# Kernel tuning notes

Measured on AMD Instinct MI355X. Metric: run time of the kernel, lower is better.

The kernel has to match this reference:

```python
import jax, jax.numpy as jnp
import numpy as np

B, S, D, H, HD, L, P = 32, 511, 512, 8, 64, 4, 501
PD = 32
FD = D - 2 * PD  # feature_proj output dim = hidden - 2*player_dim
DFF = 4 * D


def _pe(T, d):
    pos = jnp.arange(T, dtype=jnp.float32)[:, None]
    div = jnp.exp(jnp.arange(0, d, 2, dtype=jnp.float32) * (-np.log(10000.0) / d))
    pe = jnp.zeros((T, d), jnp.float32)
    pe = pe.at[:, 0::2].set(jnp.sin(pos * div))
    pe = pe.at[:, 1::2].set(jnp.cos(pos * div))
    return pe


def _ln(x, g, b, eps=1e-5):
    mu = x.mean(-1, keepdims=True)
    v = jnp.mean((x - mu) ** 2, -1, keepdims=True)
    return (x - mu) * jax.lax.rsqrt(v + eps) * g + b


def _forward(runs, wickets, overs, batters, bowlers, player_embed, Wf, bf,
             query_token, Wq, bq, Wk, bk, Wv, bv, Wo, bo,
             rec_s, bow_s, bat_s, W1, b1, W2, b2, g1, be1, g2, be2, Wout, bout):
    Bt, St = runs.shape
    T = St + 1
    # ball embedding: [B,S,3]@[3,FD] cat player embeds -> [B,S,D]
    feats = jnp.stack([runs, wickets, overs], -1) @ Wf + bf
    x = jnp.concatenate([feats, player_embed[batters], player_embed[bowlers]], -1)
    # append learned query token, add sinusoidal PE
    x = jnp.concatenate([x, jnp.broadcast_to(query_token, (Bt, 1, D))], 1)
    x = x + _pe(T, D)[None]
    # actor masks, padded with ones for the query row/col -> [B,T,T]
    sb = (bowlers[:, :, None] == bowlers[:, None, :]).astype(x.dtype)
    sm = (batters[:, :, None] == batters[:, None, :]).astype(x.dtype)
    row = jnp.ones((Bt, 1, St), x.dtype)
    col = jnp.ones((Bt, T, 1), x.dtype)
    sb = jnp.concatenate([jnp.concatenate([sb, row], 1), col], 2)
    sm = jnp.concatenate([jnp.concatenate([sm, row], 1), col], 2)
    causal = jnp.triu(jnp.ones((T, T), bool), 1)
    rec = jnp.arange(T, dtype=x.dtype) / T  # recency bias over key positions
    scale = 1.0 / np.float32(np.sqrt(HD))
    for l in range(L):
        q = (x @ Wq[l] + bq[l]).reshape(Bt, T, H, HD).transpose(0, 2, 1, 3)
        k = (x @ Wk[l] + bk[l]).reshape(Bt, T, H, HD).transpose(0, 2, 1, 3)
        v = (x @ Wv[l] + bv[l]).reshape(Bt, T, H, HD).transpose(0, 2, 1, 3)
        scores = jnp.einsum('bhqd,bhkd->bhqk', q, k) * scale
        # specialized head biases (num_heads >= 3)
        scores = scores.at[:, 0].add((rec_s[l] * rec)[None, None, :])
        scores = scores.at[:, 1].add(bow_s[l] * sb)
        scores = scores.at[:, 2].add(bat_s[l] * sm)
        scores = jnp.where(causal[None, None], -jnp.inf, scores)
        a = jax.nn.softmax(scores, axis=-1)
        o = jnp.einsum('bhqk,bhkd->bhqd', a, v).transpose(0, 2, 1, 3).reshape(Bt, T, D)
        x = _ln(x + o @ Wo[l] + bo[l], g1[l], be1[l])
        ff = jax.nn.gelu(x @ W1[l] + b1[l], approximate=False) @ W2[l] + b2[l]
        x = _ln(x + ff, g2[l], be2[l])
    return x[:, -1] @ Wout + bout  # [B, D]


def setup_inputs() -> dict:
    key = jax.random.key(0)
    ks = jax.random.split(key, 16)
    w = lambda k, sh: (0.02 * jax.random.normal(k, sh)).astype(jnp.float32)
    return {
        'runs': jax.random.uniform(ks[0], (B, S), jnp.float32),
        'wickets': jax.random.uniform(ks[1], (B, S), jnp.float32),
        'overs': jax.random.uniform(ks[2], (B, S), jnp.float32),
        'batters': jax.random.randint(ks[3], (B, S), 0, 500, jnp.int32),
        'bowlers': jax.random.randint(ks[4], (B, S), 0, 500, jnp.int32),
        'player_embed': w(ks[5], (P, PD)),
        'Wf': w(ks[6], (3, FD)), 'bf': jnp.zeros((FD,), jnp.float32),
        'query_token': jax.random.normal(ks[7], (1, 1, D), jnp.float32),
        'Wq': w(ks[8], (L, D, D)), 'bq': jnp.zeros((L, D), jnp.float32),
        'Wk': w(ks[9], (L, D, D)), 'bk': jnp.zeros((L, D), jnp.float32),
        'Wv': w(ks[10], (L, D, D)), 'bv': jnp.zeros((L, D), jnp.float32),
        'Wo': w(ks[11], (L, D, D)), 'bo': jnp.zeros((L, D), jnp.float32),
        'rec_s': jnp.full((L,), 0.5, jnp.float32),
        'bow_s': jnp.full((L,), 2.0, jnp.float32),
        'bat_s': jnp.full((L,), 2.0, jnp.float32),
        'W1': w(ks[12], (L, D, DFF)), 'b1': jnp.zeros((L, DFF), jnp.float32),
        'W2': w(ks[13], (L, DFF, D)), 'b2': jnp.zeros((L, D), jnp.float32),
        'g1': jnp.ones((L, D), jnp.float32), 'be1': jnp.zeros((L, D), jnp.float32),
        'g2': jnp.ones((L, D), jnp.float32), 'be2': jnp.zeros((L, D), jnp.float32),
        'Wout': w(ks[14], (D, D)), 'bout': jnp.zeros((D,), jnp.float32),
    }


def reference(runs, wickets, overs, batters, bowlers, player_embed, Wf, bf,
              query_token, Wq, bq, Wk, bk, Wv, bv, Wo, bo,
              rec_s, bow_s, bat_s, W1, b1, W2, b2, g1, be1, g2, be2, Wout, bout):
    return _forward(runs, wickets, overs, batters, bowlers, player_embed, Wf, bf,
                    query_token, Wq, bq, Wk, bk, Wv, bv, Wo, bo,
                    rec_s, bow_s, bat_s, W1, b1, W2, b2, g1, be1, g2, be2, Wout, bout)
```

## Files before the change

kernel.cpp:

```cpp
#include <hip/hip_runtime.h>
#include <math.h>

#define B_ 32
#define S_ 511
#define T_ 512
#define D_ 512
#define H_ 8
#define HD_ 64
#define L_ 4
#define P_ 501
#define PD_ 32
#define FD_ 448
#define DFF_ 2048

typedef __attribute__((ext_vector_type(8))) short bf16x8;
typedef __attribute__((ext_vector_type(4))) float f32x4;

__device__ __forceinline__ unsigned short f2bf(float f) {
  union { float f; unsigned int u; } c; c.f = f;
  unsigned int r = c.u + 0x7FFFu + ((c.u >> 16) & 1u);
  return (unsigned short)(r >> 16);
}

__global__ __launch_bounds__(256) void wtrans_kernel(
    const float* __restrict__ in, unsigned short* __restrict__ out, int K, int N)
{
  __shared__ float t[64][65];
  const int l = blockIdx.z;
  in  += (size_t)l * K * N;
  out += (size_t)l * N * K;
  const int k0 = blockIdx.x * 64, n0 = blockIdx.y * 64;
  const int tx = threadIdx.x & 63, ty = threadIdx.x >> 6;
#pragma unroll
  for (int i = 0; i < 16; ++i) {
    int r = ty + i * 4;
    t[r][tx] = in[(size_t)(k0 + r) * N + n0 + tx];
  }
  __syncthreads();
#pragma unroll
  for (int i = 0; i < 16; ++i) {
    int r = ty + i * 4;
    out[(size_t)(n0 + r) * K + k0 + tx] = f2bf(t[tx][r]);
  }
}

__global__ __launch_bounds__(256) void embed_kernel(
    const float* __restrict__ runs, const float* __restrict__ wickets,
    const float* __restrict__ overs, const int* __restrict__ batters,
    const int* __restrict__ bowlers, const float* __restrict__ pemb,
    const float* __restrict__ Wf, const float* __restrict__ bfv,
    const float* __restrict__ qtok, float* __restrict__ x,
    unsigned short* __restrict__ xb)
{
  size_t idx = (size_t)blockIdx.x * 256 + threadIdx.x;
  const size_t total = (size_t)B_ * T_ * D_;
  if (idx >= total) return;
  int d = (int)(idx % D_);
  int t = (int)((idx / D_) % T_);
  int b = (int)(idx / ((size_t)D_ * T_));
  float val;
  if (t < S_) {
    size_t st = (size_t)b * S_ + t;
    if (d < FD_) {
      val = runs[st] * Wf[d] + wickets[st] * Wf[FD_ + d] + overs[st] * Wf[2 * FD_ + d] + bfv[d];
    } else if (d < FD_ + PD_) {
      val = pemb[(size_t)batters[st] * PD_ + (d - FD_)];
    } else {
      val = pemb[(size_t)bowlers[st] * PD_ + (d - FD_ - PD_)];
    }
  } else {
    val = qtok[d];
  }
  float div = expf((float)(2 * (d >> 1)) * (-9.210340371976184f / (float)D_));
  float ang = (float)t * div;
  val += (d & 1) ? cosf(ang) : sinf(ang);
  x[idx] = val;
  xb[idx] = f2bf(val);
}

template<int ACT>
__global__ __launch_bounds__(256) void mfma_gemm(
    const unsigned short* __restrict__ A, const unsigned short* __restrict__ Bt,
    const float* __restrict__ bias, float* __restrict__ C,
    unsigned short* __restrict__ Cb, int N, int K)
{
  __shared__ unsigned short As[128 * 32];
  __shared__ unsigned short Bs[128 * 32];
  const int tid = threadIdx.x;
  const int m0 = blockIdx.y * 128, n0 = blockIdx.x * 128;
  const int lane = tid & 63, w = tid >> 6;
  const int wr = w >> 1, wc = w & 1;
  const int lr = lane & 15, lg = lane >> 4;

  f32x4 acc[4][4] = {};

  const int sr = tid >> 2, sc8 = (tid & 3) * 8;
  const unsigned short* gA = A + (size_t)(m0 + sr) * K + sc8;
  const unsigned short* gB = Bt + (size_t)(n0 + sr) * K + sc8;
  const size_t rowK64 = (size_t)64 * K;

  for (int k0 = 0; k0 < K; k0 += 32) {
    __syncthreads();
    *(bf16x8*)&As[sr * 32 + sc8]        = *(const bf16x8*)(gA + k0);
    *(bf16x8*)&As[(sr + 64) * 32 + sc8] = *(const bf16x8*)(gA + rowK64 + k0);
    *(bf16x8*)&Bs[sr * 32 + sc8]        = *(const bf16x8*)(gB + k0);
    *(bf16x8*)&Bs[(sr + 64) * 32 + sc8] = *(const bf16x8*)(gB + rowK64 + k0);
    __syncthreads();
    bf16x8 af[4], bfr[4];
#pragma unroll
    for (int f = 0; f < 4; ++f) {
      af[f]  = *(const bf16x8*)&As[(wr * 64 + f * 16 + lr) * 32 + lg * 8];
      bfr[f] = *(const bf16x8*)&Bs[(wc * 64 + f * 16 + lr) * 32 + lg * 8];
    }
#pragma unroll
    for (int i = 0; i < 4; ++i)
#pragma unroll
      for (int j = 0; j < 4; ++j)
        acc[i][j] = __builtin_amdgcn_mfma_f32_16x16x32_bf16(af[i], bfr[j], acc[i][j], 0, 0, 0);
  }

  const int crow0 = m0 + wr * 64 + lg * 4;
  const int ccol0 = n0 + wc * 64 + lr;
#pragma unroll
  for (int i = 0; i < 4; ++i) {
#pragma unroll
    for (int j = 0; j < 4; ++j) {
      const int col = ccol0 + j * 16;
      const float bcol = bias[col];
#pragma unroll
      for (int r = 0; r < 4; ++r) {
        const int row = crow0 + i * 16 + r;
        float v = acc[i][j][r] + bcol;
        if (ACT == 1) {
          v = 0.5f * v * (1.0f + erff(v * 0.70710678118654752f));
          Cb[(size_t)row * N + col] = f2bf(v);
        } else if (ACT == 2) {
          Cb[(size_t)row * N + col] = f2bf(v);
        } else {
          C[(size_t)row * N + col] = v;
        }
      }
    }
  }
}

__global__ __launch_bounds__(256) void vtrans_kernel(
    const unsigned short* __restrict__ vb, unsigned short* __restrict__ vt)
{
  __shared__ unsigned short tile[64 * 65];
  const int t0 = blockIdx.x * 64, h = blockIdx.y, b = blockIdx.z;
  const int tid = threadIdx.x;
  const int r = tid >> 2, ch = (tid & 3) * 16;
  const unsigned short* src = vb + ((size_t)b * T_ + t0 + r) * D_ + h * HD_ + ch;
  *(bf16x8*)&tile[r * 65 + ch]     = *(const bf16x8*)src;
  *(bf16x8*)&tile[r * 65 + ch + 8] = *(const bf16x8*)(src + 8);
  __syncthreads();
  unsigned short tmp[16];
#pragma unroll
  for (int j = 0; j < 16; ++j) tmp[j] = tile[(ch + j) * 65 + r];
  unsigned short* dst = vt + ((size_t)(b * H_ + h) * HD_ + r) * T_ + t0 + ch;
  *(bf16x8*)dst       = *(const bf16x8*)&tmp[0];
  *(bf16x8*)(dst + 8) = *(const bf16x8*)&tmp[8];
}

__global__ __launch_bounds__(256) void flash_mfma_kernel(
    const unsigned short* __restrict__ q, const unsigned short* __restrict__ k,
    const unsigned short* __restrict__ vt, unsigned short* __restrict__ o,
    const int* __restrict__ batters, const int* __restrict__ bowlers,
    const float* __restrict__ rec_sp, const float* __restrict__ bow_sp,
    const float* __restrict__ bat_sp, int l)
{
  __shared__ unsigned short QPs[64 * 70];
  __shared__ unsigned short Ks[64 * 70];
  __shared__ unsigned short Vs[64 * 70];
  __shared__ int aq_s[64], ak_s[64];

  const int qt = blockIdx.x, h = blockIdx.y, b = blockIdx.z;
  const int tid = threadIdx.x;
  const int w = tid >> 6, lane = tid & 63;
  const int c = lane & 15, g = lane >> 4;
  const int q0 = qt * 64;

  int mode = 0; float hs = 0.f;
  if (h == 0) { mode = 1; hs = rec_sp[l]; }
  else if (h == 1) { mode = 2; hs = bow_sp[l]; }
  else if (h == 2) { mode = 3; hs = bat_sp[l]; }
  const int* actors = (mode == 2) ? bowlers : batters;

  {
    const int r = tid >> 2, ch = (tid & 3) * 16;
    const unsigned short* src = q + ((size_t)b * T_ + q0 + r) * D_ + h * HD_ + ch;
    *(bf16x8*)&QPs[r * 70 + ch]     = *(const bf16x8*)src;
    *(bf16x8*)&QPs[r * 70 + ch + 8] = *(const bf16x8*)(src + 8);
  }
  if (tid < 64) {
    int qg_ = q0 + tid;
    aq_s[tid] = (mode >= 2 && qg_ < S_) ? actors[(size_t)b * S_ + qg_] : -1;
  }
  __syncthreads();

  bf16x8 af0 = *(const bf16x8*)&QPs[(w * 16 + c) * 70 + g * 8];
  bf16x8 af1 = *(const bf16x8*)&QPs[(w * 16 + c) * 70 + 32 + g * 8];

  int aq4[4];
#pragma unroll
  for (int r = 0; r < 4; ++r) aq4[r] = aq_s[w * 16 + 4 * g + r];

  float m_r[4] = {-INFINITY, -INFINITY, -INFINITY, -INFINITY};
  float l_r[4] = {0.f, 0.f, 0.f, 0.f};
  f32x4 o_acc[4] = {};

  for (int kt = 0; kt <= qt; ++kt) {
    const int k0 = kt * 64;
    __syncthreads();
    {
      const int r = tid >> 2, ch = (tid & 3) * 16;
      const unsigned short* ksrc = k + ((size_t)b * T_ + k0 + r) * D_ + h * HD_ + ch;
      *(bf16x8*)&Ks[r * 70 + ch]     = *(const bf16x8*)ksrc;
      *(bf16x8*)&Ks[r * 70 + ch + 8] = *(const bf16x8*)(ksrc + 8);
      const unsigned short* vsrc = vt + ((size_t)(b * H_ + h) * HD_ + r) * T_ + k0 + ch;
      *(bf16x8*)&Vs[r * 70 + ch]     = *(const bf16x8*)vsrc;
      *(bf16x8*)&Vs[r * 70 + ch + 8] = *(const bf16x8*)(vsrc + 8);
    }
    if (tid < 64) {
      int kg_ = k0 + tid;
      ak_s[tid] = (mode >= 2 && kg_ < S_) ? actors[(size_t)b * S_ + kg_] : -1;
    }
    __syncthreads();

    f32x4 s[4] = {};
#pragma unroll
    for (int f = 0; f < 4; ++f) {
      bf16x8 b0 = *(const bf16x8*)&Ks[(f * 16 + c) * 70 + g * 8];
      bf16x8 b1 = *(const bf16x8*)&Ks[(f * 16 + c) * 70 + 32 + g * 8];
      s[f] = __builtin_amdgcn_mfma_f32_16x16x32_bf16(af0, b0, s[f], 0, 0, 0);
      s[f] = __builtin_amdgcn_mfma_f32_16x16x32_bf16(af1, b1, s[f], 0, 0, 0);
    }

    int ak4[4];
#pragma unroll
    for (int f = 0; f < 4; ++f) ak4[f] = ak_s[f * 16 + c];
    float sv[4][4];
#pragma unroll
    for (int f = 0; f < 4; ++f) {
      const int kg = k0 + f * 16 + c;
#pragma unroll
      for (int r = 0; r < 4; ++r) {
        const int qg = q0 + w * 16 + 4 * g + r;
        float val = s[f][r] * 0.125f;
        if (mode == 1) {
          val = fmaf(hs, (float)kg * (1.0f / (float)T_), val);
        } else if (mode >= 2) {
          float eq = (qg == S_ || kg == S_) ? 1.0f : ((aq4[r] == ak4[f]) ? 1.0f : 0.0f);
          val = fmaf(hs, eq, val);
        }
        if (kg > qg) val = -INFINITY;
        sv[f][r] = val;
      }
    }

    float cr[4], rs[4];
#pragma unroll
    for (int r = 0; r < 4; ++r) {
      float pm = fmaxf(fmaxf(sv[0][r], sv[1][r]), fmaxf(sv[2][r], sv[3][r]));
      pm = fmaxf(pm, __shfl_xor(pm, 1));
      pm = fmaxf(pm, __shfl_xor(pm, 2));
      pm = fmaxf(pm, __shfl_xor(pm, 4));
      pm = fmaxf(pm, __shfl_xor(pm, 8));
      float m_new = fmaxf(m_r[r], pm);
      cr[r] = __expf(m_r[r] - m_new);
      m_r[r] = m_new;
      rs[r] = 0.f;
    }
#pragma unroll
    for (int f = 0; f < 4; ++f) {
#pragma unroll
      for (int r = 0; r < 4; ++r) {
        float p = __expf(sv[f][r] - m_r[r]);
        rs[r] += p;
        QPs[(w * 16 + 4 * g + r) * 70 + f * 16 + c] = f2bf(p);
      }
    }
#pragma unroll
    for (int r = 0; r < 4; ++r) {
      float t = rs[r];
      t += __shfl_xor(t, 1);
      t += __shfl_xor(t, 2);
      t += __shfl_xor(t, 4);
      t += __shfl_xor(t, 8);
      l_r[r] = l_r[r] * cr[r] + t;
#pragma unroll
      for (int f = 0; f < 4; ++f) o_acc[f][r] *= cr[r];
    }

    bf16x8 pa0 = *(const bf16x8*)&QPs[(w * 16 + c) * 70 + g * 8];
    bf16x8 pa1 = *(const bf16x8*)&QPs[(w * 16 + c) * 70 + 32 + g * 8];
#pragma unroll
    for (int f = 0; f < 4; ++f) {
      bf16x8 v0 = *(const bf16x8*)&Vs[(f * 16 + c) * 70 + g * 8];
      bf16x8 v1 = *(const bf16x8*)&Vs[(f * 16 + c) * 70 + 32 + g * 8];
      o_acc[f] = __builtin_amdgcn_mfma_f32_16x16x32_bf16(pa0, v0, o_acc[f], 0, 0, 0);
      o_acc[f] = __builtin_amdgcn_mfma_f32_16x16x32_bf16(pa1, v1, o_acc[f], 0, 0, 0);
    }
  }

  float inv[4];
#pragma unroll
  for (int r = 0; r < 4; ++r) inv[r] = 1.0f / l_r[r];
#pragma unroll
  for (int f = 0; f < 4; ++f) {
#pragma unroll
    for (int r = 0; r < 4; ++r) {
      const int row = q0 + w * 16 + 4 * g + r;
      o[((size_t)b * T_ + row) * D_ + h * HD_ + f * 16 + c] = f2bf(o_acc[f][r] * inv[r]);
    }
  }
}

__global__ __launch_bounds__(256) void add_ln_kernel(
    float* __restrict__ x, const float* __restrict__ y,
    const float* __restrict__ g, const float* __restrict__ be,
    unsigned short* __restrict__ xb)
{
  int row = blockIdx.x;
  int tid = threadIdx.x;
  size_t base = (size_t)row * D_;
  float v0 = x[base + tid] + y[base + tid];
  float v1 = x[base + tid + 256] + y[base + tid + 256];
  float s = v0 + v1;
  float s2 = v0 * v0 + v1 * v1;
  __shared__ float redA[4], redB[4];
#pragma unroll
  for (int off = 32; off > 0; off >>= 1) {
    s  += __shfl_down(s, off);
    s2 += __shfl_down(s2, off);
  }
  if ((tid & 63) == 0) { redA[tid >> 6] = s; redB[tid >> 6] = s2; }
  __syncthreads();
  float st  = redA[0] + redA[1] + redA[2] + redA[3];
  float s2t = redB[0] + redB[1] + redB[2] + redB[3];
  float mu = st * (1.0f / (float)D_);
  float var = s2t * (1.0f / (float)D_) - mu * mu;
  float r = rsqrtf(var + 1e-5f);
  float o0 = (v0 - mu) * r * g[tid] + be[tid];
  float o1 = (v1 - mu) * r * g[tid + 256] + be[tid + 256];
  x[base + tid]        = o0;
  x[base + tid + 256]  = o1;
  xb[base + tid]       = f2bf(o0);
  xb[base + tid + 256] = f2bf(o1);
}

__global__ __launch_bounds__(256) void final_kernel(
    const float* __restrict__ x, const float* __restrict__ Wout,
    const float* __restrict__ bout, float* __restrict__ out)
{
  __shared__ float xs[D_];
  int b = blockIdx.x;
  int n = blockIdx.y * 256 + threadIdx.x;
  const float* xr = x + ((size_t)b * T_ + (T_ - 1)) * D_;
  xs[threadIdx.x] = xr[threadIdx.x];
  xs[threadIdx.x + 256] = xr[threadIdx.x + 256];
  __syncthreads();
  float acc = bout[n];
  for (int kk = 0; kk < D_; ++kk)
    acc = fmaf(xs[kk], Wout[(size_t)kk * D_ + n], acc);
  out[(size_t)b * D_ + n] = acc;
}

extern "C" void kernel_launch(void* const* d_in, const int* in_sizes, int n_in,
                              void* d_out, int out_size, void* d_ws, size_t ws_size,
                              hipStream_t stream)
{
  const float* runs    = (const float*)d_in[0];
  const float* wickets = (const float*)d_in[1];
  const float* overs   = (const float*)d_in[2];
  const int*   batters = (const int*)d_in[3];
  const int*   bowlers = (const int*)d_in[4];
  const float* pemb    = (const float*)d_in[5];
  const float* Wf      = (const float*)d_in[6];
  const float* bfv     = (const float*)d_in[7];
  const float* qtok    = (const float*)d_in[8];
  const float* Wq      = (const float*)d_in[9];
  const float* bq      = (const float*)d_in[10];
  const float* Wk      = (const float*)d_in[11];
  const float* bk      = (const float*)d_in[12];
  const float* Wv      = (const float*)d_in[13];
  const float* bv      = (const float*)d_in[14];
  const float* Wo      = (const float*)d_in[15];
  const float* bo      = (const float*)d_in[16];
  const float* rec_s   = (const float*)d_in[17];
  const float* bow_s   = (const float*)d_in[18];
  const float* bat_s   = (const float*)d_in[19];
  const float* W1      = (const float*)d_in[20];
  const float* b1      = (const float*)d_in[21];
  const float* W2      = (const float*)d_in[22];
  const float* b2      = (const float*)d_in[23];
  const float* g1      = (const float*)d_in[24];
  const float* be1     = (const float*)d_in[25];
  const float* g2      = (const float*)d_in[26];
  const float* be2     = (const float*)d_in[27];
  const float* Wout    = (const float*)d_in[28];
  const float* bout    = (const float*)d_in[29];

  float* ws = (float*)d_ws;
  const size_t n1 = (size_t)B_ * T_ * D_;
  float* x  = ws;
  float* yb = ws + n1;
  unsigned short* xb   = (unsigned short*)(ws + 2 * n1);
  unsigned short* qb16 = xb + n1;
  unsigned short* kb16 = qb16 + n1;
  unsigned short* vb16 = kb16 + n1;
  unsigned short* vt   = vb16 + n1;
  unsigned short* ob   = vt + n1;
  unsigned short* wt   = ob + n1;
  unsigned short* hb   = qb16;

  const size_t wsz = (size_t)L_ * D_ * D_;
  unsigned short* wtq = wt;
  unsigned short* wtk = wtq + wsz;
  unsigned short* wtv = wtk + wsz;
  unsigned short* wto = wtv + wsz;
  unsigned short* wt1 = wto + wsz;
  unsigned short* wt2 = wt1 + (size_t)L_ * D_ * DFF_;

  const int M = B_ * T_;
  dim3 blk(256);

  wtrans_kernel<<<dim3(8, 8, L_),  blk, 0, stream>>>(Wq, wtq, D_, D_);
  wtrans_kernel<<<dim3(8, 8, L_),  blk, 0, stream>>>(Wk, wtk, D_, D_);
  wtrans_kernel<<<dim3(8, 8, L_),  blk, 0, stream>>>(Wv, wtv, D_, D_);
  wtrans_kernel<<<dim3(8, 8, L_),  blk, 0, stream>>>(Wo, wto, D_, D_);
  wtrans_kernel<<<dim3(8, 32, L_), blk, 0, stream>>>(W1, wt1, D_, DFF_);
  wtrans_kernel<<<dim3(32, 8, L_), blk, 0, stream>>>(W2, wt2, DFF_, D_);

  {
    size_t total = (size_t)B_ * T_ * D_;
    int nb = (int)((total + 255) / 256);
    embed_kernel<<<nb, blk, 0, stream>>>(runs, wickets, overs, batters, bowlers,
                                         pemb, Wf, bfv, qtok, x, xb);
  }

  for (int l = 0; l < L_; ++l) {
    mfma_gemm<2><<<dim3(D_ / 128, M / 128), blk, 0, stream>>>(
        xb, wtq + (size_t)l * D_ * D_, bq + l * D_, nullptr, qb16, D_, D_);
    mfma_gemm<2><<<dim3(D_ / 128, M / 128), blk, 0, stream>>>(
        xb, wtk + (size_t)l * D_ * D_, bk + l * D_, nullptr, kb16, D_, D_);
    mfma_gemm<2><<<dim3(D_ / 128, M / 128), blk, 0, stream>>>(
        xb, wtv + (size_t)l * D_ * D_, bv + l * D_, nullptr, vb16, D_, D_);

    vtrans_kernel<<<dim3(T_ / 64, H_, B_), blk, 0, stream>>>(vb16, vt);

    flash_mfma_kernel<<<dim3(T_ / 64, H_, B_), blk, 0, stream>>>(
        qb16, kb16, vt, ob, batters, bowlers, rec_s, bow_s, bat_s, l);

    mfma_gemm<0><<<dim3(D_ / 128, M / 128), blk, 0, stream>>>(
        ob, wto + (size_t)l * D_ * D_, bo + l * D_, yb, nullptr, D_, D_);
    add_ln_kernel<<<M, blk, 0, stream>>>(x, yb, g1 + l * D_, be1 + l * D_, xb);

    mfma_gemm<1><<<dim3(DFF_ / 128, M / 128), blk, 0, stream>>>(
        xb, wt1 + (size_t)l * D_ * DFF_, b1 + l * DFF_, nullptr, hb, DFF_, D_);
    mfma_gemm<0><<<dim3(D_ / 128, M / 128), blk, 0, stream>>>(
        hb, wt2 + (size_t)l * DFF_ * D_, b2 + l * D_, yb, nullptr, D_, DFF_);
    add_ln_kernel<<<M, blk, 0, stream>>>(x, yb, g2 + l * D_, be2 + l * D_, xb);
  }

  final_kernel<<<dim3(B_, D_ / 256), blk, 0, stream>>>(x, Wout, bout, (float*)d_out);
}
```

Before: 1.540 ms.

## Use direct-to-LDS GEMM loads, fuse V transpose, widen flash query tile

The GEMM now stages A and B tiles with global_load_lds, copying straight from global memory into shared memory, and moves the barrier to the end of each k-step. The V projection GEMM writes its output already transposed per head, which removes the separate vtrans kernel and its extra round trip through memory. The flash attention kernel handles 128 query rows per block, with two 16-row subtiles per wave, so each K/V tile loaded is reused by twice as many rows. Waves whose rows lie entirely above the causal diagonal skip the compute. In exchange, the transposed V store is scattered (strided), the attention grid has half as many blocks, and the heavier causal blocks are less evenly balanced.

```diff
diff --git a/kernel.cpp b/kernel.cpp
--- a/kernel.cpp
+++ b/kernel.cpp
@@ -15,6 +15,10 @@
 
 typedef __attribute__((ext_vector_type(8))) short bf16x8;
 typedef __attribute__((ext_vector_type(4))) float f32x4;
+
+#define GLDS16(gp, lp) __builtin_amdgcn_global_load_lds(                      \
+    (const __attribute__((address_space(1))) void*)(gp),                      \
+    (__attribute__((address_space(3))) void*)(lp), 16, 0, 0)
 
 __device__ __forceinline__ unsigned short f2bf(float f) {
   union { float f; unsigned int u; } c; c.f = f;
@@ -94,17 +98,22 @@
 
   f32x4 acc[4][4] = {};
 
-  const int sr = tid >> 2, sc8 = (tid & 3) * 8;
-  const unsigned short* gA = A + (size_t)(m0 + sr) * K + sc8;
-  const unsigned short* gB = Bt + (size_t)(n0 + sr) * K + sc8;
-  const size_t rowK64 = (size_t)64 * K;
+  const int srow = w * 16 + (lane >> 2);
+  const int sc8 = (lane & 3) * 8;
+  const unsigned short* gA0 = A + (size_t)(m0 + srow) * K + sc8;
+  const unsigned short* gA1 = gA0 + (size_t)64 * K;
+  const unsigned short* gB0 = Bt + (size_t)(n0 + srow) * K + sc8;
+  const unsigned short* gB1 = gB0 + (size_t)64 * K;
+  unsigned short* lA0 = &As[(w * 16) * 32];
+  unsigned short* lA1 = &As[(64 + w * 16) * 32];
+  unsigned short* lB0 = &Bs[(w * 16) * 32];
+  unsigned short* lB1 = &Bs[(64 + w * 16) * 32];
 
   for (int k0 = 0; k0 < K; k0 += 32) {
-    __syncthreads();
-    *(bf16x8*)&As[sr * 32 + sc8]        = *(const bf16x8*)(gA + k0);
-    *(bf16x8*)&As[(sr + 64) * 32 + sc8] = *(const bf16x8*)(gA + rowK64 + k0);
-    *(bf16x8*)&Bs[sr * 32 + sc8]        = *(const bf16x8*)(gB + k0);
-    *(bf16x8*)&Bs[(sr + 64) * 32 + sc8] = *(const bf16x8*)(gB + rowK64 + k0);
+    GLDS16(gA0 + k0, lA0);
+    GLDS16(gA1 + k0, lA1);
+    GLDS16(gB0 + k0, lB0);
+    GLDS16(gB1 + k0, lB1);
     __syncthreads();
     bf16x8 af[4], bfr[4];
 #pragma unroll
@@ -117,6 +126,7 @@
 #pragma unroll
       for (int j = 0; j < 4; ++j)
         acc[i][j] = __builtin_amdgcn_mfma_f32_16x16x32_bf16(af[i], bfr[j], acc[i][j], 0, 0, 0);
+    __syncthreads();
   }
 
   const int crow0 = m0 + wr * 64 + lg * 4;
@@ -136,31 +146,16 @@
           Cb[(size_t)row * N + col] = f2bf(v);
         } else if (ACT == 2) {
           Cb[(size_t)row * N + col] = f2bf(v);
+        } else if (ACT == 3) {
+          const int t = row & (T_ - 1), bb = row >> 9;
+          const int hh = col >> 6, hd = col & 63;
+          Cb[(((size_t)bb * H_ + hh) * HD_ + hd) * T_ + t] = f2bf(v);
         } else {
           C[(size_t)row * N + col] = v;
         }
       }
     }
   }
-}
-
-__global__ __launch_bounds__(256) void vtrans_kernel(
-    const unsigned short* __restrict__ vb, unsigned short* __restrict__ vt)
-{
-  __shared__ unsigned short tile[64 * 65];
-  const int t0 = blockIdx.x * 64, h = blockIdx.y, b = blockIdx.z;
-  const int tid = threadIdx.x;
-  const int r = tid >> 2, ch = (tid & 3) * 16;
-  const unsigned short* src = vb + ((size_t)b * T_ + t0 + r) * D_ + h * HD_ + ch;
-  *(bf16x8*)&tile[r * 65 + ch]     = *(const bf16x8*)src;
-  *(bf16x8*)&tile[r * 65 + ch + 8] = *(const bf16x8*)(src + 8);
-  __syncthreads();
-  unsigned short tmp[16];
-#pragma unroll
-  for (int j = 0; j < 16; ++j) tmp[j] = tile[(ch + j) * 65 + r];
-  unsigned short* dst = vt + ((size_t)(b * H_ + h) * HD_ + r) * T_ + t0 + ch;
-  *(bf16x8*)dst       = *(const bf16x8*)&tmp[0];
-  *(bf16x8*)(dst + 8) = *(const bf16x8*)&tmp[8];
 }
 
 __global__ __launch_bounds__(256) void flash_mfma_kernel(
@@ -170,16 +165,16 @@
     const float* __restrict__ rec_sp, const float* __restrict__ bow_sp,
     const float* __restrict__ bat_sp, int l)
 {
-  __shared__ unsigned short QPs[64 * 70];
+  __shared__ unsigned short QPs[128 * 70];
   __shared__ unsigned short Ks[64 * 70];
   __shared__ unsigned short Vs[64 * 70];
-  __shared__ int aq_s[64], ak_s[64];
+  __shared__ int aq_s[128], ak_s[64];
 
   const int qt = blockIdx.x, h = blockIdx.y, b = blockIdx.z;
   const int tid = threadIdx.x;
   const int w = tid >> 6, lane = tid & 63;
   const int c = lane & 15, g = lane >> 4;
-  const int q0 = qt * 64;
+  const int q0 = qt * 128;
 
   int mode = 0; float hs = 0.f;
   if (h == 0) { mode = 1; hs = rec_sp[l]; }
@@ -187,40 +182,50 @@
   else if (h == 2) { mode = 3; hs = bat_sp[l]; }
   const int* actors = (mode == 2) ? bowlers : batters;
 
-  {
-    const int r = tid >> 2, ch = (tid & 3) * 16;
-    const unsigned short* src = q + ((size_t)b * T_ + q0 + r) * D_ + h * HD_ + ch;
-    *(bf16x8*)&QPs[r * 70 + ch]     = *(const bf16x8*)src;
-    *(bf16x8*)&QPs[r * 70 + ch + 8] = *(const bf16x8*)(src + 8);
-  }
-  if (tid < 64) {
+  const int sr = tid >> 2, sch = (tid & 3) * 16;
+
+#pragma unroll
+  for (int half = 0; half < 2; ++half) {
+    const unsigned short* src = q + ((size_t)b * T_ + q0 + half * 64 + sr) * D_ + h * HD_ + sch;
+    *(bf16x8*)&QPs[(half * 64 + sr) * 70 + sch]     = *(const bf16x8*)src;
+    *(bf16x8*)&QPs[(half * 64 + sr) * 70 + sch + 8] = *(const bf16x8*)(src + 8);
+  }
+  if (tid < 128) {
     int qg_ = q0 + tid;
     aq_s[tid] = (mode >= 2 && qg_ < S_) ? actors[(size_t)b * S_ + qg_] : -1;
   }
   __syncthreads();
 
-  bf16x8 af0 = *(const bf16x8*)&QPs[(w * 16 + c) * 70 + g * 8];
-  bf16x8 af1 = *(const bf16x8*)&QPs[(w * 16 + c) * 70 + 32 + g * 8];
-
-  int aq4[4];
-#pragma unroll
-  for (int r = 0; r < 4; ++r) aq4[r] = aq_s[w * 16 + 4 * g + r];
-
-  float m_r[4] = {-INFINITY, -INFINITY, -INFINITY, -INFINITY};
-  float l_r[4] = {0.f, 0.f, 0.f, 0.f};
-  f32x4 o_acc[4] = {};
-
-  for (int kt = 0; kt <= qt; ++kt) {
+  bf16x8 af[2][2];
+#pragma unroll
+  for (int m = 0; m < 2; ++m) {
+    af[m][0] = *(const bf16x8*)&QPs[(w * 32 + m * 16 + c) * 70 + g * 8];
+    af[m][1] = *(const bf16x8*)&QPs[(w * 32 + m * 16 + c) * 70 + 32 + g * 8];
+  }
+  int aq4[2][4];
+#pragma unroll
+  for (int m = 0; m < 2; ++m)
+#pragma unroll
+    for (int r = 0; r < 4; ++r) aq4[m][r] = aq_s[w * 32 + m * 16 + 4 * g + r];
+
+  float m_r[2][4], l_r[2][4];
+#pragma unroll
+  for (int m = 0; m < 2; ++m)
+#pragma unroll
+    for (int r = 0; r < 4; ++r) { m_r[m][r] = -INFINITY; l_r[m][r] = 0.f; }
+  f32x4 o_acc[2][4] = {};
+
+  const int ktmax = 2 * qt + 1;
+  for (int kt = 0; kt <= ktmax; ++kt) {
     const int k0 = kt * 64;
     __syncthreads();
     {
-      const int r = tid >> 2, ch = (tid & 3) * 16;
-      const unsigned short* ksrc = k + ((size_t)b * T_ + k0 + r) * D_ + h * HD_ + ch;
-      *(bf16x8*)&Ks[r * 70 + ch]     = *(const bf16x8*)ksrc;
-      *(bf16x8*)&Ks[r * 70 + ch + 8] = *(const bf16x8*)(ksrc + 8);
-      const unsigned short* vsrc = vt + ((size_t)(b * H_ + h) * HD_ + r) * T_ + k0 + ch;
-      *(bf16x8*)&Vs[r * 70 + ch]     = *(const bf16x8*)vsrc;
-      *(bf16x8*)&Vs[r * 70 + ch + 8] = *(const bf16x8*)(vsrc + 8);
+      const unsigned short* ksrc = k + ((size_t)b * T_ + k0 + sr) * D_ + h * HD_ + sch;
+      *(bf16x8*)&Ks[sr * 70 + sch]     = *(const bf16x8*)ksrc;
+      *(bf16x8*)&Ks[sr * 70 + sch + 8] = *(const bf16x8*)(ksrc + 8);
+      const unsigned short* vsrc = vt + ((size_t)(b * H_ + h) * HD_ + sr) * T_ + k0 + sch;
+      *(bf16x8*)&Vs[sr * 70 + sch]     = *(const bf16x8*)vsrc;
+      *(bf16x8*)&Vs[sr * 70 + sch + 8] = *(const bf16x8*)(vsrc + 8);
     }
     if (tid < 64) {
       int kg_ = k0 + tid;
@@ -228,91 +233,106 @@
     }
     __syncthreads();
 
-    f32x4 s[4] = {};
+    if (q0 + w * 32 + 31 < k0) continue;
+
+    f32x4 s[2][4] = {};
 #pragma unroll
     for (int f = 0; f < 4; ++f) {
       bf16x8 b0 = *(const bf16x8*)&Ks[(f * 16 + c) * 70 + g * 8];
       bf16x8 b1 = *(const bf16x8*)&Ks[(f * 16 + c) * 70 + 32 + g * 8];
-      s[f] = __builtin_amdgcn_mfma_f32_16x16x32_bf16(af0, b0, s[f], 0, 0, 0);
-      s[f] = __builtin_amdgcn_mfma_f32_16x16x32_bf16(af1, b1, s[f], 0, 0, 0);
+#pragma unroll
+      for (int m = 0; m < 2; ++m) {
+        s[m][f] = __builtin_amdgcn_mfma_f32_16x16x32_bf16(af[m][0], b0, s[m][f], 0, 0, 0);
+        s[m][f] = __builtin_amdgcn_mfma_f32_16x16x32_bf16(af[m][1], b1, s[m][f], 0, 0, 0);
+      }
     }
 
     int ak4[4];
 #pragma unroll
     for (int f = 0; f < 4; ++f) ak4[f] = ak_s[f * 16 + c];
-    float sv[4][4];
-#pragma unroll
-    for (int f = 0; f < 4; ++f) {
-      const int kg = k0 + f * 16 + c;
+
+#pragma unroll
+    for (int m = 0; m < 2; ++m) {
+      float sv[4][4];
+#pragma unroll
+      for (int f = 0; f < 4; ++f) {
+        const int kg = k0 + f * 16 + c;
+#pragma unroll
+        for (int r = 0; r < 4; ++r) {
+          const int qg = q0 + w * 32 + m * 16 + 4 * g + r;
+          float val = s[m][f][r] * 0.125f;
+          if (mode == 1) {
+            val = fmaf(hs, (float)kg * (1.0f / (float)T_), val);
+          } else if (mode >= 2) {
+            float eq = (qg == S_ || kg == S_) ? 1.0f : ((aq4[m][r] == ak4[f]) ? 1.0f : 0.0f);
+            val = fmaf(hs, eq, val);
+          }
+          if (kg > qg) val = -INFINITY;
+          sv[f][r] = val;
+        }
+      }
+      float cr[4];
 #pragma unroll
       for (int r = 0; r < 4; ++r) {
-        const int qg = q0 + w * 16 + 4 * g + r;
-        float val = s[f][r] * 0.125f;
-        if (mode == 1) {
-          val = fmaf(hs, (float)kg * (1.0f / (float)T_), val);
-        } else if (mode >= 2) {
-          float eq = (qg == S_ || kg == S_) ? 1.0f : ((aq4[r] == ak4[f]) ? 1.0f : 0.0f);
-          val = fmaf(hs, eq, val);
+        float pm = fmaxf(fmaxf(sv[0][r], sv[1][r]), fmaxf(sv[2][r], sv[3][r]));
+        pm = fmaxf(pm, __shfl_xor(pm, 1));
+        pm = fmaxf(pm, __shfl_xor(pm, 2));
+        pm = fmaxf(pm, __shfl_xor(pm, 4));
+        pm = fmaxf(pm, __shfl_xor(pm, 8));
+        float m_new = fmaxf(m_r[m][r], pm);
+        cr[r] = __expf(m_r[m][r] - m_new);
+        m_r[m][r] = m_new;
+      }
+      float rs[4] = {0.f, 0.f, 0.f, 0.f};
+#pragma unroll
+      for (int f = 0; f < 4; ++f) {
+#pragma unroll
+        for (int r = 0; r < 4; ++r) {
+          float p = __expf(sv[f][r] - m_r[m][r]);
+          rs[r] += p;
+          QPs[(w * 32 + m * 16 + 4 * g + r) * 70 + f * 16 + c] = f2bf(p);
         }
-        if (kg > qg) val = -INFINITY;
-        sv[f][r] = val;
-      }
-    }
-
-    float cr[4], rs[4];
-#pragma unroll
-    for (int r = 0; r < 4; ++r) {
-      float pm = fmaxf(fmaxf(sv[0][r], sv[1][r]), fmaxf(sv[2][r], sv[3][r]));
-      pm = fmaxf(pm, __shfl_xor(pm, 1));
-      pm = fmaxf(pm, __shfl_xor(pm, 2));
-      pm = fmaxf(pm, __shfl_xor(pm, 4));
-      pm = fmaxf(pm, __shfl_xor(pm, 8));
-      float m_new = fmaxf(m_r[r], pm);
-      cr[r] = __expf(m_r[r] - m_new);
-      m_r[r] = m_new;
-      rs[r] = 0.f;
-    }
-#pragma unroll
-    for (int f = 0; f < 4; ++f) {
+      }
 #pragma unroll
       for (int r = 0; r < 4; ++r) {
-        float p = __expf(sv[f][r] - m_r[r]);
-        rs[r] += p;
-        QPs[(w * 16 + 4 * g + r) * 70 + f * 16 + c] = f2bf(p);
-      }
-    }
-#pragma unroll
-    for (int r = 0; r < 4; ++r) {
-      float t = rs[r];
-      t += __shfl_xor(t, 1);
-      t += __shfl_xor(t, 2);
-      t += __shfl_xor(t, 4);
-      t += __shfl_xor(t, 8);
-      l_r[r] = l_r[r] * cr[r] + t;
-#pragma unroll
-      for (int f = 0; f < 4; ++f) o_acc[f][r] *= cr[r];
-    }
-
-    bf16x8 pa0 = *(const bf16x8*)&QPs[(w * 16 + c) * 70 + g * 8];
-    bf16x8 pa1 = *(const bf16x8*)&QPs[(w * 16 + c) * 70 + 32 + g * 8];
+        float t = rs[r];
+        t += __shfl_xor(t, 1);
+        t += __shfl_xor(t, 2);
+        t += __shfl_xor(t, 4);
+        t += __shfl_xor(t, 8);
+        l_r[m][r] = l_r[m][r] * cr[r] + t;
+#pragma unroll
+        for (int f = 0; f < 4; ++f) o_acc[m][f][r] *= cr[r];
+      }
+    }
+
+    bf16x8 pa[2][2];
+#pragma unroll
+    for (int m = 0; m < 2; ++m) {
+      pa[m][0] = *(const bf16x8*)&QPs[(w * 32 + m * 16 + c) * 70 + g * 8];
+      pa[m][1] = *(const bf16x8*)&QPs[(w * 32 + m * 16 + c) * 70 + 32 + g * 8];
+    }
 #pragma unroll
     for (int f = 0; f < 4; ++f) {
       bf16x8 v0 = *(const bf16x8*)&Vs[(f * 16 + c) * 70 + g * 8];
       bf16x8 v1 = *(const bf16x8*)&Vs[(f * 16 + c) * 70 + 32 + g * 8];
-      o_acc[f] = __builtin_amdgcn_mfma_f32_16x16x32_bf16(pa0, v0, o_acc[f], 0, 0, 0);
-      o_acc[f] = __builtin_amdgcn_mfma_f32_16x16x32_bf16(pa1, v1, o_acc[f], 0, 0, 0);
-    }
-  }
-
-  float inv[4];
-#pragma unroll
-  for (int r = 0; r < 4; ++r) inv[r] = 1.0f / l_r[r];
-#pragma unroll
-  for (int f = 0; f < 4; ++f) {
+#pragma unroll
+      for (int m = 0; m < 2; ++m) {
+        o_acc[m][f] = __builtin_amdgcn_mfma_f32_16x16x32_bf16(pa[m][0], v0, o_acc[m][f], 0, 0, 0);
+        o_acc[m][f] = __builtin_amdgcn_mfma_f32_16x16x32_bf16(pa[m][1], v1, o_acc[m][f], 0, 0, 0);
+      }
+    }
+  }
+
+#pragma unroll
+  for (int m = 0; m < 2; ++m) {
 #pragma unroll
     for (int r = 0; r < 4; ++r) {
-      const int row = q0 + w * 16 + 4 * g + r;
-      o[((size_t)b * T_ + row) * D_ + h * HD_ + f * 16 + c] = f2bf(o_acc[f][r] * inv[r]);
+      const float inv = 1.0f / l_r[m][r];
+      const int row = q0 + w * 32 + m * 16 + 4 * g + r;
+#pragma unroll
+      for (int f = 0; f < 4; ++f)
+        o[((size_t)b * T_ + row) * D_ + h * HD_ + f * 16 + c] = f2bf(o_acc[m][f][r] * inv);
     }
   }
 }
@@ -445,12 +465,10 @@
         xb, wtq + (size_t)l * D_ * D_, bq + l * D_, nullptr, qb16, D_, D_);
     mfma_gemm<2><<<dim3(D_ / 128, M / 128), blk, 0, stream>>>(
         xb, wtk + (size_t)l * D_ * D_, bk + l * D_, nullptr, kb16, D_, D_);
-    mfma_gemm<2><<<dim3(D_ / 128, M / 128), blk, 0, stream>>>(
-        xb, wtv + (size_t)l * D_ * D_, bv + l * D_, nullptr, vb16, D_, D_);
-
-    vtrans_kernel<<<dim3(T_ / 64, H_, B_), blk, 0, stream>>>(vb16, vt);
-
-    flash_mfma_kernel<<<dim3(T_ / 64, H_, B_), blk, 0, stream>>>(
+    mfma_gemm<3><<<dim3(D_ / 128, M / 128), blk, 0, stream>>>(
+        xb, wtv + (size_t)l * D_ * D_, bv + l * D_, nullptr, vt, D_, D_);
+
+    flash_mfma_kernel<<<dim3(T_ / 128, H_, B_), blk, 0, stream>>>(
         qb16, kb16, vt, ob, batters, bowlers, rec_s, bow_s, bat_s, l);
 
     mfma_gemm<0><<<dim3(D_ / 128, M / 128), blk, 0, stream>>>(
```

Result: no change. 1.554 ms (+0.9%).
